# Performance work log

Hardware: AMD Instinct MI355X
Metric: run time of the kernel (lower is better)

The kernel has to match this reference:

```python
import jax, jax.numpy as jnp
import numpy as np

TAU = 1.0  # FLAGS.tau


def setup_inputs() -> dict:
    key = jax.random.key(0)
    k1, k2, k3, k4 = jax.random.split(key, 4)
    B, N, E, D_in, D_out = 64, 512, 8, 64, 64
    edge_features = jax.random.normal(k1, (B, N, N, E), dtype=jnp.float32)
    x = jax.random.normal(k2, (B * N, D_in), dtype=jnp.float32)
    # glorot init for weights, normal for coef (as in source)
    lim = np.sqrt(6.0 / (D_in + D_out))
    W = jax.random.uniform(k3, (D_in, D_out), dtype=jnp.float32, minval=-lim, maxval=lim)
    coef = jax.random.normal(k4, (E, 1), dtype=jnp.float32)
    return {"edge_features": edge_features, "x": x, "W": W, "coef": coef}


def reference(edge_features, x, W, coef):
    B, N, _, E = edge_features.shape
    D_out = W.shape[1]
    # node transform: [B*N, D_in] @ [D_in, D_out]
    pre_sup = (x @ W).reshape(B, N, D_out)
    # per-edge attention score: [B,N,N,E] @ [E,1] -> [B,N,N]
    scores = jnp.einsum('bije,e->bij', edge_features, coef[:, 0])
    adj = jax.nn.softmax(scores / TAU, axis=-1)
    # preprocess_adj: add self-loops, symmetric D^-1/2 (A+I) D^-1/2.
    # Block-diagonal structure means normalization is per-graph, so we stay batched
    # instead of materializing the [B*N, B*N] block-diagonal matrix.
    adj_hat = adj + jnp.eye(N, dtype=adj.dtype)
    d_inv_sqrt = jax.lax.rsqrt(adj_hat.sum(axis=-1))  # [B,N]
    adj_norm = adj_hat * d_inv_sqrt[:, :, None] * d_inv_sqrt[:, None, :]
    # adjacency-weighted aggregation (block-diagonal matmul == batched matmul)
    out = jnp.einsum('bij,bjd->bid', adj_norm, pre_sup).reshape(B * N, D_out)
    return jax.nn.relu(out)
```

## Files before the change

kernel.cpp:

```cpp
#include <hip/hip_runtime.h>
#include <math.h>

#define B_  64
#define N_  512
#define E_  8
#define D_  64
#define TI  4

typedef float f32x4 __attribute__((ext_vector_type(4)));

__global__ __launch_bounds__(256) void presup_kernel(
    const float* __restrict__ x, const float* __restrict__ W, float* __restrict__ ps)
{
    __shared__ float Wl[64 * 64];
    const int t = threadIdx.x;
#pragma unroll
    for (int i = 0; i < 4; ++i)
        ((f32x4*)Wl)[t + i * 256] = ((const f32x4*)W)[t + i * 256];
    __syncthreads();

    const int d4  = (t & 15) * 4;
    const int r   = t >> 4;
    const int row = blockIdx.x * 16 + r;
    const float* xr = x + (size_t)row * 64;

    f32x4 acc = 0.f;
#pragma unroll
    for (int k = 0; k < 64; k += 4) {
        f32x4 xv = *(const f32x4*)&xr[k];
        f32x4 w0 = *(const f32x4*)&Wl[(k + 0) * 64 + d4];
        f32x4 w1 = *(const f32x4*)&Wl[(k + 1) * 64 + d4];
        f32x4 w2 = *(const f32x4*)&Wl[(k + 2) * 64 + d4];
        f32x4 w3 = *(const f32x4*)&Wl[(k + 3) * 64 + d4];
        acc += xv.x * w0;
        acc += xv.y * w1;
        acc += xv.z * w2;
        acc += xv.w * w3;
    }
    *(f32x4*)&ps[(size_t)row * 64 + d4] = acc;
}

__global__ __launch_bounds__(256) void fused_kernel(
    const float* __restrict__ edge, const float* __restrict__ coef,
    const float* __restrict__ ps, float* __restrict__ out)
{
    __shared__ alignas(16) float s4[N_][TI];
    __shared__ float denom[TI];
    __shared__ alignas(16) float part[16][TI * 64];

    const int t  = threadIdx.x;
    const int b  = blockIdx.x >> 7;
    const int i0 = (blockIdx.x & 127) * TI;

    const float c0 = coef[0], c1 = coef[1], c2 = coef[2], c3 = coef[3];
    const float c4 = coef[4], c5 = coef[5], c6 = coef[6], c7 = coef[7];

    {
        const size_t rowbase = ((size_t)b * N_ + i0) * (size_t)(N_ * E_);
#pragma unroll
        for (int r = 0; r < TI; ++r) {
#pragma unroll
            for (int jj = 0; jj < 2; ++jj) {
                const int j = t + jj * 256;
                const f32x4* ep = (const f32x4*)(edge + rowbase
                                    + (size_t)r * (N_ * E_) + (size_t)j * E_);
                f32x4 e0 = __builtin_nontemporal_load(ep);
                f32x4 e1 = __builtin_nontemporal_load(ep + 1);
                s4[j][r] = e0.x * c0 + e0.y * c1 + e0.z * c2 + e0.w * c3
                         + e1.x * c4 + e1.y * c5 + e1.z * c6 + e1.w * c7;
            }
        }
    }
    __syncthreads();

    {
        const int w = t >> 6, l = t & 63;
        float m = -INFINITY;
#pragma unroll
        for (int k = 0; k < N_ / 64; ++k) m = fmaxf(m, s4[l + k * 64][w]);
#pragma unroll
        for (int off = 32; off; off >>= 1) m = fmaxf(m, __shfl_xor(m, off, 64));
        float sum = 0.f;
#pragma unroll
        for (int k = 0; k < N_ / 64; ++k) {
            float p = __expf(s4[l + k * 64][w] - m);
            s4[l + k * 64][w] = p;
            sum += p;
        }
#pragma unroll
        for (int off = 32; off; off >>= 1) sum += __shfl_xor(sum, off, 64);
        if (l == 0) denom[w] = sum;
    }
    __syncthreads();

    const int d4 = (t & 15) * 4;
    const int jg = t >> 4;
    const float* psb = ps + (size_t)b * (N_ * D_);

    f32x4 a0 = 0.f, a1 = 0.f, a2 = 0.f, a3 = 0.f;
#pragma unroll 4
    for (int k = 0; k < N_ / 16; ++k) {
        const int j = jg + (k << 4);
        f32x4 v  = *(const f32x4*)&psb[j * D_ + d4];
        f32x4 pv = *(const f32x4*)&s4[j][0];
        a0 += pv.x * v;
        a1 += pv.y * v;
        a2 += pv.z * v;
        a3 += pv.w * v;
    }
    *(f32x4*)&part[jg][0 * 64 + d4] = a0;
    *(f32x4*)&part[jg][1 * 64 + d4] = a1;
    *(f32x4*)&part[jg][2 * 64 + d4] = a2;
    *(f32x4*)&part[jg][3 * 64 + d4] = a3;
    __syncthreads();

    {
        const int r2 = t >> 6, d = t & 63;
        float sum = 0.f;
#pragma unroll
        for (int g = 0; g < 16; ++g) sum += part[g][t];
        const int row = i0 + r2;
        const float val = 0.5f * (sum / denom[r2] + psb[row * D_ + d]);
        out[((size_t)b * N_ + row) * D_ + d] = fmaxf(val, 0.f);
    }
}

extern "C" void kernel_launch(void* const* d_in, const int* in_sizes, int n_in,
                              void* d_out, int out_size, void* d_ws, size_t ws_size,
                              hipStream_t stream) {
    const float* edge = (const float*)d_in[0];
    const float* x    = (const float*)d_in[1];
    const float* W    = (const float*)d_in[2];
    const float* coef = (const float*)d_in[3];
    float* out = (float*)d_out;
    float* ps  = (float*)d_ws;

    presup_kernel<<<(B_ * N_) / 16, 256, 0, stream>>>(x, W, ps);
    fused_kernel<<<B_ * (N_ / TI), 256, 0, stream>>>(edge, coef, ps, out);
}
```

Baseline: 151.3 us.

## Double rows per block and reuse pre_sup loads across eight rows

```diff
diff --git a/kernel.cpp b/kernel.cpp
--- a/kernel.cpp
+++ b/kernel.cpp
@@ -5,7 +5,7 @@
 #define N_  512
 #define E_  8
 #define D_  64
-#define TI  4
+#define TI  8
 
 typedef float f32x4 __attribute__((ext_vector_type(4)));
 
@@ -44,13 +44,13 @@
     const float* __restrict__ edge, const float* __restrict__ coef,
     const float* __restrict__ ps, float* __restrict__ out)
 {
-    __shared__ alignas(16) float s4[N_][TI];
+    __shared__ alignas(16) float s4t[TI][N_];
+    __shared__ alignas(16) float part[4][TI * D_];
     __shared__ float denom[TI];
-    __shared__ alignas(16) float part[16][TI * 64];
 
     const int t  = threadIdx.x;
-    const int b  = blockIdx.x >> 7;
-    const int i0 = (blockIdx.x & 127) * TI;
+    const int b  = blockIdx.x >> 6;
+    const int i0 = (blockIdx.x & 63) * TI;
 
     const float c0 = coef[0], c1 = coef[1], c2 = coef[2], c3 = coef[3];
     const float c4 = coef[4], c5 = coef[5], c6 = coef[6], c7 = coef[7];
@@ -66,8 +66,8 @@
                                     + (size_t)r * (N_ * E_) + (size_t)j * E_);
                 f32x4 e0 = __builtin_nontemporal_load(ep);
                 f32x4 e1 = __builtin_nontemporal_load(ep + 1);
-                s4[j][r] = e0.x * c0 + e0.y * c1 + e0.z * c2 + e0.w * c3
-                         + e1.x * c4 + e1.y * c5 + e1.z * c6 + e1.w * c7;
+                s4t[r][j] = e0.x * c0 + e0.y * c1 + e0.z * c2 + e0.w * c3
+                          + e1.x * c4 + e1.y * c5 + e1.z * c6 + e1.w * c7;
             }
         }
     }
@@ -75,21 +75,27 @@
 
     {
         const int w = t >> 6, l = t & 63;
-        float m = -INFINITY;
 #pragma unroll
-        for (int k = 0; k < N_ / 64; ++k) m = fmaxf(m, s4[l + k * 64][w]);
+        for (int rr = 0; rr < 2; ++rr) {
+            const int row = w * 2 + rr;
+            f32x4 v0 = *(const f32x4*)&s4t[row][l * 4];
+            f32x4 v1 = *(const f32x4*)&s4t[row][l * 4 + 256];
+            float m = fmaxf(fmaxf(fmaxf(v0.x, v0.y), fmaxf(v0.z, v0.w)),
+                            fmaxf(fmaxf(v1.x, v1.y), fmaxf(v1.z, v1.w)));
 #pragma unroll
-        for (int off = 32; off; off >>= 1) m = fmaxf(m, __shfl_xor(m, off, 64));
-        float sum = 0.f;
+            for (int off = 32; off; off >>= 1) m = fmaxf(m, __shfl_xor(m, off, 64));
+            v0.x = __expf(v0.x - m); v0.y = __expf(v0.y - m);
+            v0.z = __expf(v0.z - m); v0.w = __expf(v0.w - m);
+            v1.x = __expf(v1.x - m); v1.y = __expf(v1.y - m);
+            v1.z = __expf(v1.z - m); v1.w = __expf(v1.w - m);
+            *(f32x4*)&s4t[row][l * 4]       = v0;
+            *(f32x4*)&s4t[row][l * 4 + 256] = v1;
+            float sum = (v0.x + v0.y) + (v0.z + v0.w)
+                      + (v1.x + v1.y) + (v1.z + v1.w);
 #pragma unroll
-        for (int k = 0; k < N_ / 64; ++k) {
-            float p = __expf(s4[l + k * 64][w] - m);
-            s4[l + k * 64][w] = p;
-            sum += p;
+            for (int off = 32; off; off >>= 1) sum += __shfl_xor(sum, off, 64);
+            if (l == 0) denom[row] = sum;
         }
-#pragma unroll
-        for (int off = 32; off; off >>= 1) sum += __shfl_xor(sum, off, 64);
-        if (l == 0) denom[w] = sum;
     }
     __syncthreads();
 
@@ -97,31 +103,54 @@
     const int jg = t >> 4;
     const float* psb = ps + (size_t)b * (N_ * D_);
 
-    f32x4 a0 = 0.f, a1 = 0.f, a2 = 0.f, a3 = 0.f;
-#pragma unroll 4
-    for (int k = 0; k < N_ / 16; ++k) {
-        const int j = jg + (k << 4);
-        f32x4 v  = *(const f32x4*)&psb[j * D_ + d4];
-        f32x4 pv = *(const f32x4*)&s4[j][0];
-        a0 += pv.x * v;
-        a1 += pv.y * v;
-        a2 += pv.z * v;
-        a3 += pv.w * v;
+    f32x4 acc[TI];
+#pragma unroll
+    for (int r = 0; r < TI; ++r) acc[r] = 0.f;
+
+#pragma unroll 2
+    for (int k = 0; k < N_ / 64; ++k) {
+        const int j0 = jg * 4 + k * 64;
+        f32x4 v0 = *(const f32x4*)&psb[(j0 + 0) * D_ + d4];
+        f32x4 v1 = *(const f32x4*)&psb[(j0 + 1) * D_ + d4];
+        f32x4 v2 = *(const f32x4*)&psb[(j0 + 2) * D_ + d4];
+        f32x4 v3 = *(const f32x4*)&psb[(j0 + 3) * D_ + d4];
+#pragma unroll
+        for (int r = 0; r < TI; ++r) {
+            f32x4 pv = *(const f32x4*)&s4t[r][j0];
+            acc[r] += pv.x * v0;
+            acc[r] += pv.y * v1;
+            acc[r] += pv.z * v2;
+            acc[r] += pv.w * v3;
+        }
     }
-    *(f32x4*)&part[jg][0 * 64 + d4] = a0;
-    *(f32x4*)&part[jg][1 * 64 + d4] = a1;
-    *(f32x4*)&part[jg][2 * 64 + d4] = a2;
-    *(f32x4*)&part[jg][3 * 64 + d4] = a3;
+
+#pragma unroll
+    for (int r = 0; r < TI; ++r) {
+#pragma unroll
+        for (int c4 = 0; c4 < 4; ++c4) {
+            float v = acc[r][c4];
+            v += __shfl_xor(v, 16, 64);
+            v += __shfl_xor(v, 32, 64);
+            acc[r][c4] = v;
+        }
+    }
+    const int w = t >> 6;
+    if ((t & 48) == 0) {
+#pragma unroll
+        for (int r = 0; r < TI; ++r)
+            *(f32x4*)&part[w][r * D_ + d4] = acc[r];
+    }
     __syncthreads();
 
-    {
-        const int r2 = t >> 6, d = t & 63;
-        float sum = 0.f;
 #pragma unroll
-        for (int g = 0; g < 16; ++g) sum += part[g][t];
-        const int row = i0 + r2;
-        const float val = 0.5f * (sum / denom[r2] + psb[row * D_ + d]);
-        out[((size_t)b * N_ + row) * D_ + d] = fmaxf(val, 0.f);
+    for (int u = 0; u < 2; ++u) {
+        const int idx = t + u * 256;
+        const int r = idx >> 6, d = idx & 63;
+        float sum = part[0][idx] + part[1][idx] + part[2][idx] + part[3][idx];
+        const int row = i0 + r;
+        const float val = 0.5f * (sum / denom[r] + psb[row * D_ + d]);
+        __builtin_nontemporal_store(fmaxf(val, 0.f),
+                                    &out[((size_t)b * N_ + row) * D_ + d]);
     }
 }
 
```

Result: no change. 153.7 us (+1.6%).

## Stream softmax-aggregation per wave over 8 rows without max subtraction

Applied to the files above, without the earlier changes.

```diff
diff --git a/kernel.cpp b/kernel.cpp
--- a/kernel.cpp
+++ b/kernel.cpp
@@ -5,7 +5,8 @@
 #define N_  512
 #define E_  8
 #define D_  64
-#define TI  4
+#define RG  8
+#define WV  4
 
 typedef float f32x4 __attribute__((ext_vector_type(4)));
 
@@ -40,88 +41,67 @@
     *(f32x4*)&ps[(size_t)row * 64 + d4] = acc;
 }
 
-__global__ __launch_bounds__(256) void fused_kernel(
+__global__ __launch_bounds__(256, 4) void fused_kernel(
     const float* __restrict__ edge, const float* __restrict__ coef,
     const float* __restrict__ ps, float* __restrict__ out)
 {
-    __shared__ alignas(16) float s4[N_][TI];
-    __shared__ float denom[TI];
-    __shared__ alignas(16) float part[16][TI * 64];
+    __shared__ alignas(16) float pl[WV][64][RG];
 
-    const int t  = threadIdx.x;
-    const int b  = blockIdx.x >> 7;
-    const int i0 = (blockIdx.x & 127) * TI;
+    const int t = threadIdx.x, w = t >> 6, l = t & 63;
+    const int blk  = blockIdx.x;
+    const int b    = blk >> 4;
+    const int row0 = (blk & 15) * (WV * RG) + w * RG;
 
     const float c0 = coef[0], c1 = coef[1], c2 = coef[2], c3 = coef[3];
     const float c4 = coef[4], c5 = coef[5], c6 = coef[6], c7 = coef[7];
 
-    {
-        const size_t rowbase = ((size_t)b * N_ + i0) * (size_t)(N_ * E_);
+    const float* eb  = edge + (((size_t)b * N_ + row0) * N_ + l) * E_;
+    const float* psb = ps + (size_t)b * (N_ * D_);
+
+    float acc[RG], lsum[RG];
 #pragma unroll
-        for (int r = 0; r < TI; ++r) {
+    for (int r = 0; r < RG; ++r) { acc[r] = 0.f; lsum[r] = 0.f; }
+
+    for (int c = 0; c < N_ / 64; ++c) {
+        const int j0 = c * 64;
+
+        f32x4 pv0, pv1;
 #pragma unroll
-            for (int jj = 0; jj < 2; ++jj) {
-                const int j = t + jj * 256;
-                const f32x4* ep = (const f32x4*)(edge + rowbase
-                                    + (size_t)r * (N_ * E_) + (size_t)j * E_);
-                f32x4 e0 = __builtin_nontemporal_load(ep);
-                f32x4 e1 = __builtin_nontemporal_load(ep + 1);
-                s4[j][r] = e0.x * c0 + e0.y * c1 + e0.z * c2 + e0.w * c3
-                         + e1.x * c4 + e1.y * c5 + e1.z * c6 + e1.w * c7;
-            }
+        for (int r = 0; r < RG; ++r) {
+            const f32x4* ep = (const f32x4*)(eb + ((size_t)r * N_ + j0) * E_);
+            f32x4 e0 = __builtin_nontemporal_load(ep);
+            f32x4 e1 = __builtin_nontemporal_load(ep + 1);
+            float s = e0.x * c0 + e0.y * c1 + e0.z * c2 + e0.w * c3
+                    + e1.x * c4 + e1.y * c5 + e1.z * c6 + e1.w * c7;
+            float p = __expf(s);
+            lsum[r] += p;
+            if (r < 4) pv0[r] = p; else pv1[r - 4] = p;
+        }
+        *(f32x4*)&pl[w][l][0] = pv0;
+        *(f32x4*)&pl[w][l][4] = pv1;
+
+#pragma unroll 8
+        for (int j = 0; j < 64; ++j) {
+            f32x4 pa = *(const f32x4*)&pl[w][j][0];
+            f32x4 pb = *(const f32x4*)&pl[w][j][4];
+            float v  = psb[(size_t)(j0 + j) * D_ + l];
+            acc[0] += pa.x * v;  acc[1] += pa.y * v;
+            acc[2] += pa.z * v;  acc[3] += pa.w * v;
+            acc[4] += pb.x * v;  acc[5] += pb.y * v;
+            acc[6] += pb.z * v;  acc[7] += pb.w * v;
         }
     }
-    __syncthreads();
 
-    {
-        const int w = t >> 6, l = t & 63;
-        float m = -INFINITY;
 #pragma unroll
-        for (int k = 0; k < N_ / 64; ++k) m = fmaxf(m, s4[l + k * 64][w]);
+    for (int r = 0; r < RG; ++r) {
+        float s = lsum[r];
 #pragma unroll
-        for (int off = 32; off; off >>= 1) m = fmaxf(m, __shfl_xor(m, off, 64));
-        float sum = 0.f;
-#pragma unroll
-        for (int k = 0; k < N_ / 64; ++k) {
-            float p = __expf(s4[l + k * 64][w] - m);
-            s4[l + k * 64][w] = p;
-            sum += p;
-        }
-#pragma unroll
-        for (int off = 32; off; off >>= 1) sum += __shfl_xor(sum, off, 64);
-        if (l == 0) denom[w] = sum;
-    }
-    __syncthreads();
-
-    const int d4 = (t & 15) * 4;
-    const int jg = t >> 4;
-    const float* psb = ps + (size_t)b * (N_ * D_);
-
-    f32x4 a0 = 0.f, a1 = 0.f, a2 = 0.f, a3 = 0.f;
-#pragma unroll 4
-    for (int k = 0; k < N_ / 16; ++k) {
-        const int j = jg + (k << 4);
-        f32x4 v  = *(const f32x4*)&psb[j * D_ + d4];
-        f32x4 pv = *(const f32x4*)&s4[j][0];
-        a0 += pv.x * v;
-        a1 += pv.y * v;
-        a2 += pv.z * v;
-        a3 += pv.w * v;
-    }
-    *(f32x4*)&part[jg][0 * 64 + d4] = a0;
-    *(f32x4*)&part[jg][1 * 64 + d4] = a1;
-    *(f32x4*)&part[jg][2 * 64 + d4] = a2;
-    *(f32x4*)&part[jg][3 * 64 + d4] = a3;
-    __syncthreads();
-
-    {
-        const int r2 = t >> 6, d = t & 63;
-        float sum = 0.f;
-#pragma unroll
-        for (int g = 0; g < 16; ++g) sum += part[g][t];
-        const int row = i0 + r2;
-        const float val = 0.5f * (sum / denom[r2] + psb[row * D_ + d]);
-        out[((size_t)b * N_ + row) * D_ + d] = fmaxf(val, 0.f);
+        for (int off = 32; off; off >>= 1) s += __shfl_xor(s, off, 64);
+        const int row = row0 + r;
+        const float self = psb[(size_t)row * D_ + l];
+        const float val  = 0.5f * (acc[r] / s + self);
+        __builtin_nontemporal_store(fmaxf(val, 0.f),
+                                    &out[((size_t)b * N_ + row) * D_ + l]);
     }
 }
 
@@ -136,5 +116,5 @@
     float* ps  = (float*)d_ws;
 
     presup_kernel<<<(B_ * N_) / 16, 256, 0, stream>>>(x, W, ps);
-    fused_kernel<<<B_ * (N_ / TI), 256, 0, stream>>>(edge, coef, ps, out);
+    fused_kernel<<<B_ * N_ / (WV * RG), 256, 0, stream>>>(edge, coef, ps, out);
 }
```

Measured after the change: 150.9 us. About the same (-0.3%).
